# Optimization experiments

Hardware: AMD Instinct MI355X
Metric: run time of the kernel (lower is better)

The kernel has to match this reference:

```python
import jax, jax.numpy as jnp
import numpy as np

N = 100000          # nodes
E = 1600000         # edges
NODE_DIM = 128
EDGE_DIM = 1
EMB = 16            # out_channels per head
H = 2               # heads
HID = 32
OUT = 2
NEG_SLOPE = 0.2


def gatv2_layer(x, src, dst, eattr, Wl, bl, Wr, br, We, att, bias):
    """PyG GATv2Conv: add self-loops (edge_attr fill='mean'), edge attention,
    segment softmax over target nodes, scatter-add aggregation, concat heads."""
    n = x.shape[0]
    heads, ch = att.shape
    # --- add self loops; self-loop edge_attr = mean of incoming edge_attr per node ---
    ones = jnp.ones((src.shape[0],), dtype=x.dtype)
    deg = jax.ops.segment_sum(ones, dst, num_segments=n)
    loop_attr = jax.ops.segment_sum(eattr, dst, num_segments=n) / jnp.maximum(deg, 1.0)[:, None]
    idx = jnp.arange(n, dtype=src.dtype)
    src2 = jnp.concatenate([src, idx])
    dst2 = jnp.concatenate([dst, idx])
    eattr2 = jnp.concatenate([eattr, loop_attr], axis=0)
    # --- linear projections ---
    xl = (x @ Wl + bl).reshape(n, heads, ch)   # source-side (lin_l)
    xr = (x @ Wr + br).reshape(n, heads, ch)   # target-side (lin_r)
    ef = (eattr2 @ We).reshape(-1, heads, ch)  # edge features (lin_edge, no bias)
    # --- per-edge attention logits (GATv2: LeakyReLU inside, then att dot) ---
    e = xl[src2] + xr[dst2] + ef               # [E2, H, C]
    e = jnp.where(e >= 0, e, NEG_SLOPE * e)
    logits = jnp.einsum('ehc,hc->eh', e, att)  # [E2, H]
    # --- segment softmax over edges sharing the same target node ---
    m = jax.ops.segment_max(logits, dst2, num_segments=n)      # [N, H]
    a = jnp.exp(logits - m[dst2])
    denom = jax.ops.segment_sum(a, dst2, num_segments=n)
    alpha = a / denom[dst2]                                    # [E2, H]
    # --- scatter-add weighted source messages ---
    msg = (alpha[:, :, None] * xl[src2]).reshape(-1, heads * ch)
    out = jax.ops.segment_sum(msg, dst2, num_segments=n)       # [N, H*C]
    return out + bias


def setup_inputs() -> dict:
    key = jax.random.key(0)
    ks = jax.random.split(key, 24)
    p = lambda k, s: (jax.random.normal(k, s, dtype=jnp.float32) * 0.1)
    HC = H * EMB
    return {
        'x': jax.random.normal(ks[0], (N, NODE_DIM), dtype=jnp.float32),
        'edge_index': jax.random.randint(ks[1], (2, E), 0, N, dtype=jnp.int32),
        'edge_attr': jax.random.normal(ks[2], (E, EDGE_DIM), dtype=jnp.float32),
        # layer 1
        'Wl1': p(ks[3], (NODE_DIM, HC)), 'bl1': p(ks[4], (HC,)),
        'Wr1': p(ks[5], (NODE_DIM, HC)), 'br1': p(ks[6], (HC,)),
        'We1': p(ks[7], (EDGE_DIM, HC)), 'att1': p(ks[8], (H, EMB)), 'b1': p(ks[9], (HC,)),
        # layer 2 (input dim = H*EMB)
        'Wl2': p(ks[10], (HC, HC)), 'bl2': p(ks[11], (HC,)),
        'Wr2': p(ks[12], (HC, HC)), 'br2': p(ks[13], (HC,)),
        'We2': p(ks[14], (EDGE_DIM, HC)), 'att2': p(ks[15], (H, EMB)), 'b2': p(ks[16], (HC,)),
        # decoder MLP
        'Wd1': p(ks[17], (HC, HID)), 'bd1': p(ks[18], (HID,)),
        'Wd2': p(ks[19], (HID, OUT)), 'bd2': p(ks[20], (OUT,)),
    }


def reference(x, edge_index, edge_attr,
              Wl1, bl1, Wr1, br1, We1, att1, b1,
              Wl2, bl2, Wr2, br2, We2, att2, b2,
              Wd1, bd1, Wd2, bd2):
    src, dst = edge_index[0], edge_index[1]
    h = gatv2_layer(x, src, dst, edge_attr, Wl1, bl1, Wr1, br1, We1, att1, b1)
    h = gatv2_layer(h, src, dst, edge_attr, Wl2, bl2, Wr2, br2, We2, att2, b2)
    h = jax.nn.relu(h @ Wd1 + bd1)
    return h @ Wd2 + bd2
```

## Files before the change

### kernel.cpp

```cpp
#include <hip/hip_runtime.h>
#include <hip/hip_fp16.h>
#include <math.h>


#define NN 100000
#define NE 1600000
#define SLOT 48
#define ROWU 64
#define NEG_SLOPE 0.2f

__device__ __forceinline__ float pk_ea(unsigned p) {
    return __half2float(__ushort_as_half((unsigned short)((p & 0x7FFFu) << 1)));
}
__device__ __forceinline__ float lrelu(float v) {
    return (v >= 0.f) ? v : NEG_SLOPE * v;
}

template <int K>
__global__ void proj_scatter_kernel(const float* __restrict__ x,
                                    const float* __restrict__ Wl, const float* __restrict__ bl,
                                    const float* __restrict__ Wr, const float* __restrict__ br,
                                    __half* __restrict__ xl, float* __restrict__ xr,
                                    const int* __restrict__ src, const int* __restrict__ dst,
                                    const float* __restrict__ eattr,
                                    unsigned* __restrict__ csr) {
    __shared__ __align__(16) float sWl[K * 32];
    __shared__ __align__(16) float sWr[K * 32];
    __shared__ float sb[64];
    for (int i = threadIdx.x; i < K * 32; i += blockDim.x) {
        int k = i >> 5, col = i & 31;
        int p = (((k >> 2) ^ (col & 7)) << 2) | (k & 3);
        sWl[col * K + p] = Wl[i];
        sWr[col * K + p] = Wr[i];
    }
    if (threadIdx.x < 32) sb[threadIdx.x] = bl[threadIdx.x];
    else if (threadIdx.x < 64) sb[threadIdx.x] = br[threadIdx.x - 32];
    __syncthreads();
    int t = blockIdx.x * blockDim.x + threadIdx.x;
    int g = t >> 5, col = t & 31;
    int row0 = g * 4;
    {
        const float4* x0 = (const float4*)(x + (size_t)(row0 + 0) * K);
        const float4* x1 = (const float4*)(x + (size_t)(row0 + 1) * K);
        const float4* x2 = (const float4*)(x + (size_t)(row0 + 2) * K);
        const float4* x3 = (const float4*)(x + (size_t)(row0 + 3) * K);
        const float4* wl4 = (const float4*)(sWl + col * K);
        const float4* wr4 = (const float4*)(sWr + col * K);
        int swz = col & 7;
        float al0 = 0.f, al1 = 0.f, al2 = 0.f, al3 = 0.f;
        float ar0 = 0.f, ar1 = 0.f, ar2 = 0.f, ar3 = 0.f;
#pragma unroll 4
        for (int k4 = 0; k4 < K / 4; k4++) {
            float4 wl = wl4[k4 ^ swz];
            float4 wr = wr4[k4 ^ swz];
            float4 a = x0[k4];
            float4 b = x1[k4];
            float4 c = x2[k4];
            float4 d = x3[k4];
            al0 = fmaf(a.x, wl.x, al0); al0 = fmaf(a.y, wl.y, al0);
            al0 = fmaf(a.z, wl.z, al0); al0 = fmaf(a.w, wl.w, al0);
            ar0 = fmaf(a.x, wr.x, ar0); ar0 = fmaf(a.y, wr.y, ar0);
            ar0 = fmaf(a.z, wr.z, ar0); ar0 = fmaf(a.w, wr.w, ar0);
            al1 = fmaf(b.x, wl.x, al1); al1 = fmaf(b.y, wl.y, al1);
            al1 = fmaf(b.z, wl.z, al1); al1 = fmaf(b.w, wl.w, al1);
            ar1 = fmaf(b.x, wr.x, ar1); ar1 = fmaf(b.y, wr.y, ar1);
            ar1 = fmaf(b.z, wr.z, ar1); ar1 = fmaf(b.w, wr.w, ar1);
            al2 = fmaf(c.x, wl.x, al2); al2 = fmaf(c.y, wl.y, al2);
            al2 = fmaf(c.z, wl.z, al2); al2 = fmaf(c.w, wl.w, al2);
            ar2 = fmaf(c.x, wr.x, ar2); ar2 = fmaf(c.y, wr.y, ar2);
            ar2 = fmaf(c.z, wr.z, ar2); ar2 = fmaf(c.w, wr.w, ar2);
            al3 = fmaf(d.x, wl.x, al3); al3 = fmaf(d.y, wl.y, al3);
            al3 = fmaf(d.z, wl.z, al3); al3 = fmaf(d.w, wl.w, al3);
            ar3 = fmaf(d.x, wr.x, ar3); ar3 = fmaf(d.y, wr.y, ar3);
            ar3 = fmaf(d.z, wr.z, ar3); ar3 = fmaf(d.w, wr.w, ar3);
        }
        float bls = sb[col], brs = sb[32 + col];
        xl[(size_t)(row0 + 0) * 32 + col] = __float2half_rn(al0 + bls);
        xr[(size_t)(row0 + 0) * 32 + col] = ar0 + brs;
        xl[(size_t)(row0 + 1) * 32 + col] = __float2half_rn(al1 + bls);
        xr[(size_t)(row0 + 1) * 32 + col] = ar1 + brs;
        xl[(size_t)(row0 + 2) * 32 + col] = __float2half_rn(al2 + bls);
        xr[(size_t)(row0 + 2) * 32 + col] = ar2 + brs;
        xl[(size_t)(row0 + 3) * 32 + col] = __float2half_rn(al3 + bls);
        xr[(size_t)(row0 + 3) * 32 + col] = ar3 + brs;
    }
#pragma unroll
    for (int i = 0; i < 2; i++) {
        int e = blockIdx.x * 512 + i * 256 + threadIdx.x;
        int d = dst[e];
        unsigned* row = csr + (size_t)d * ROWU;
        int pos = atomicAdd((int*)row, 1);
        if (pos < SLOT) {
            unsigned hb = __half_as_ushort(__float2half_rn(eattr[e]));
            row[4 + pos] = ((unsigned)src[e] << 15) | (hb >> 1);
        }
    }
}

__device__ __forceinline__ void gat_core4(const unsigned* __restrict__ csr,
                                          const __half* xl, const float* xr,
                                          const float* We, const float* att,
                                          const float* bias, int node, int L,
                                          float h[4]) {
    int k = L & 7, j = L >> 3;
    const unsigned* row = csr + (size_t)node * ROWU;
    int cnt = (int)row[0];
    int deg = (cnt < SLOT) ? cnt : SLOT;
    float4 we = ((const float4*)We)[k];
    float4 at = ((const float4*)att)[k];
    float4 xrc = ((const float4*)(xr + (size_t)node * 32))[k];
    ushort4 sq = ((const ushort4*)(xl + (size_t)node * 32))[k];
    float sx0 = __half2float(__ushort_as_half(sq.x));
    float sx1 = __half2float(__ushort_as_half(sq.y));
    float sx2 = __half2float(__ushort_as_half(sq.z));
    float sx3 = __half2float(__ushort_as_half(sq.w));
    float ssum = 0.f, a0 = 0.f, a1 = 0.f, a2 = 0.f, a3 = 0.f, easum = 0.f;
    unsigned pv_c = row[4 + j];
    int n1 = j + 4; if (n1 > SLOT - 1) n1 = SLOT - 1;
    unsigned pv_n = row[4 + n1];
    bool val_c = j < deg;
    int s_c = val_c ? (int)(pv_c >> 15) : 0;
    ushort4 q_c = ((const ushort4*)(xl + (size_t)s_c * 32))[k];
    for (int base = 0; base < deg; base += 4) {
        int idx = base + j;
        bool val_n = (idx + 4) < deg;
        int s_n = val_n ? (int)(pv_n >> 15) : 0;
        ushort4 q_n = ((const ushort4*)(xl + (size_t)s_n * 32))[k];
        int n2 = idx + 8; if (n2 > SLOT - 1) n2 = SLOT - 1;
        unsigned pv_n2 = row[4 + n2];
        float ea = pk_ea(pv_c);
        float x0 = __half2float(__ushort_as_half(q_c.x));
        float x1 = __half2float(__ushort_as_half(q_c.y));
        float x2 = __half2float(__ushort_as_half(q_c.z));
        float x3 = __half2float(__ushort_as_half(q_c.w));
        float p;
        p  = at.x * lrelu(fmaf(ea, we.x, x0 + xrc.x));
        p  = fmaf(at.y, lrelu(fmaf(ea, we.y, x1 + xrc.y)), p);
        p  = fmaf(at.z, lrelu(fmaf(ea, we.z, x2 + xrc.z)), p);
        p  = fmaf(at.w, lrelu(fmaf(ea, we.w, x3 + xrc.w)), p);
        p += __shfl_xor(p, 1);
        p += __shfl_xor(p, 2);
        float w = val_c ? __expf(p) : 0.f;
        ssum += w;
        easum += val_c ? ea : 0.f;
        a0 = fmaf(w, x0, a0);
        a1 = fmaf(w, x1, a1);
        a2 = fmaf(w, x2, a2);
        a3 = fmaf(w, x3, a3);
        pv_c = pv_n; pv_n = pv_n2; q_c = q_n; val_c = val_n;
    }
    ssum  += __shfl_xor(ssum, 8);   ssum  += __shfl_xor(ssum, 16);
    easum += __shfl_xor(easum, 8);  easum += __shfl_xor(easum, 16);
    a0 += __shfl_xor(a0, 8);  a0 += __shfl_xor(a0, 16);
    a1 += __shfl_xor(a1, 8);  a1 += __shfl_xor(a1, 16);
    a2 += __shfl_xor(a2, 8);  a2 += __shfl_xor(a2, 16);
    a3 += __shfl_xor(a3, 8);  a3 += __shfl_xor(a3, 16);
    {
        float ea0 = easum / fmaxf((float)cnt, 1.f);
        float p;
        p  = at.x * lrelu(fmaf(ea0, we.x, sx0 + xrc.x));
        p  = fmaf(at.y, lrelu(fmaf(ea0, we.y, sx1 + xrc.y)), p);
        p  = fmaf(at.z, lrelu(fmaf(ea0, we.z, sx2 + xrc.z)), p);
        p  = fmaf(at.w, lrelu(fmaf(ea0, we.w, sx3 + xrc.w)), p);
        p += __shfl_xor(p, 1);
        p += __shfl_xor(p, 2);
        float w = __expf(p);
        ssum += w;
        a0 = fmaf(w, sx0, a0);
        a1 = fmaf(w, sx1, a1);
        a2 = fmaf(w, sx2, a2);
        a3 = fmaf(w, sx3, a3);
    }
    float4 bq = ((const float4*)bias)[k];
    float inv = 1.f / ssum;
    h[0] = a0 * inv + bq.x;
    h[1] = a1 * inv + bq.y;
    h[2] = a2 * inv + bq.z;
    h[3] = a3 * inv + bq.w;
}

#define HBUF_FENCE() do { \
    asm volatile("s_waitcnt lgkmcnt(0)" ::: "memory"); \
    __builtin_amdgcn_sched_barrier(0); \
} while (0)

__global__ void gat1_proj2_kernel(const unsigned* __restrict__ csr,
                                  const __half* __restrict__ xl, const float* __restrict__ xr,
                                  const float* __restrict__ We, const float* __restrict__ att,
                                  const float* __restrict__ bias,
                                  const float* __restrict__ Wl2, const float* __restrict__ bl2,
                                  const float* __restrict__ Wr2, const float* __restrict__ br2,
                                  __half* __restrict__ xl2, float* __restrict__ xr2) {
    __shared__ __align__(16) float sWl[1024];
    __shared__ __align__(16) float sWr[1024];
    __shared__ float4 hbuf[8][8];
    for (int i = threadIdx.x; i < 1024; i += blockDim.x) {
        int cc = i >> 5, Lc = i & 31;
        int p = (((cc >> 2) ^ (Lc & 7)) << 2) | (cc & 3);
        sWl[Lc * 32 + p] = Wl2[i];
        sWr[Lc * 32 + p] = Wr2[i];
    }
    __syncthreads();
    int t = blockIdx.x * blockDim.x + threadIdx.x;
    int node = t >> 5, L = t & 31;
    if (node >= NN) return;
    float h[4];
    gat_core4(csr, xl, xr, We, att, bias, node, L, h);
    int nl = threadIdx.x >> 5;
    if (L < 8) hbuf[nl][L] = make_float4(h[0], h[1], h[2], h[3]);
    HBUF_FENCE();
    const float4* hv4 = hbuf[nl];
    const float4* wl4 = (const float4*)(sWl + L * 32);
    const float4* wr4 = (const float4*)(sWr + L * 32);
    int swz = L & 7;
    float al = bl2[L], ar = br2[L];
#pragma unroll
    for (int c4 = 0; c4 < 8; c4++) {
        float4 hv = hv4[c4];
        float4 wl = wl4[c4 ^ swz];
        float4 wr = wr4[c4 ^ swz];
        al = fmaf(hv.x, wl.x, al); al = fmaf(hv.y, wl.y, al);
        al = fmaf(hv.z, wl.z, al); al = fmaf(hv.w, wl.w, al);
        ar = fmaf(hv.x, wr.x, ar); ar = fmaf(hv.y, wr.y, ar);
        ar = fmaf(hv.z, wr.z, ar); ar = fmaf(hv.w, wr.w, ar);
    }
    xl2[(size_t)node * 32 + L] = __float2half_rn(al);
    xr2[(size_t)node * 32 + L] = ar;
}

__global__ void gat2_dec_kernel(const unsigned* __restrict__ csr,
                                const __half* __restrict__ xl, const float* __restrict__ xr,
                                const float* __restrict__ We, const float* __restrict__ att,
                                const float* __restrict__ bias,
                                const float* __restrict__ Wd1, const float* __restrict__ bd1,
                                const float* __restrict__ Wd2, const float* __restrict__ bd2,
                                float* __restrict__ out) {
    __shared__ __align__(16) float sWd1[1024];
    __shared__ float sWd2[64];
    __shared__ float4 hbuf[8][8];
    for (int i = threadIdx.x; i < 1024; i += blockDim.x) {
        int cc = i >> 5, Lc = i & 31;
        int p = (((cc >> 2) ^ (Lc & 7)) << 2) | (cc & 3);
        sWd1[Lc * 32 + p] = Wd1[i];
    }
    if (threadIdx.x < 64) sWd2[threadIdx.x] = Wd2[threadIdx.x];
    __syncthreads();
    int t = blockIdx.x * blockDim.x + threadIdx.x;
    int node = t >> 5, L = t & 31;
    if (node >= NN) return;
    float h[4];
    gat_core4(csr, xl, xr, We, att, bias, node, L, h);
    int nl = threadIdx.x >> 5;
    if (L < 8) hbuf[nl][L] = make_float4(h[0], h[1], h[2], h[3]);
    HBUF_FENCE();
    const float4* hv4 = hbuf[nl];
    const float4* wd4 = (const float4*)(sWd1 + L * 32);
    int swz = L & 7;
    float d1 = bd1[L];
#pragma unroll
    for (int c4 = 0; c4 < 8; c4++) {
        float4 hv = hv4[c4];
        float4 wd = wd4[c4 ^ swz];
        d1 = fmaf(hv.x, wd.x, d1); d1 = fmaf(hv.y, wd.y, d1);
        d1 = fmaf(hv.z, wd.z, d1); d1 = fmaf(hv.w, wd.w, d1);
    }
    float hid = fmaxf(d1, 0.f);
    float o0 = hid * sWd2[L * 2 + 0];
    float o1 = hid * sWd2[L * 2 + 1];
    o0 += __shfl_xor(o0, 1);   o1 += __shfl_xor(o1, 1);
    o0 += __shfl_xor(o0, 2);   o1 += __shfl_xor(o1, 2);
    o0 += __shfl_xor(o0, 4);   o1 += __shfl_xor(o1, 4);
    o0 += __shfl_xor(o0, 8);   o1 += __shfl_xor(o1, 8);
    o0 += __shfl_xor(o0, 16);  o1 += __shfl_xor(o1, 16);
    if (L == 0) {
        out[(size_t)node * 2 + 0] = o0 + bd2[0];
        out[(size_t)node * 2 + 1] = o1 + bd2[1];
    }
}

extern "C" void kernel_launch(void* const* d_in, const int* in_sizes, int n_in,
                              void* d_out, int out_size, void* d_ws, size_t ws_size,
                              hipStream_t stream) {
    const float* x     = (const float*)d_in[0];
    const int*   src   = (const int*)d_in[1];
    const int*   dst   = src + NE;
    const float* eattr = (const float*)d_in[2];
    const float* Wl1 = (const float*)d_in[3],  *bl1 = (const float*)d_in[4];
    const float* Wr1 = (const float*)d_in[5],  *br1 = (const float*)d_in[6];
    const float* We1 = (const float*)d_in[7],  *att1 = (const float*)d_in[8];
    const float* b1  = (const float*)d_in[9];
    const float* Wl2 = (const float*)d_in[10], *bl2 = (const float*)d_in[11];
    const float* Wr2 = (const float*)d_in[12], *br2 = (const float*)d_in[13];
    const float* We2 = (const float*)d_in[14], *att2 = (const float*)d_in[15];
    const float* b2  = (const float*)d_in[16];
    const float* Wd1 = (const float*)d_in[17], *bd1 = (const float*)d_in[18];
    const float* Wd2 = (const float*)d_in[19], *bd2 = (const float*)d_in[20];
    float* out = (float*)d_out;

    char* w = (char*)d_ws;
    unsigned* csr = (unsigned*)w;  w += (size_t)NN * ROWU * 4;
    __half*   xl  = (__half*)w;    w += (size_t)NN * 32 * 2;
    float*    xr  = (float*)w;     w += (size_t)NN * 32 * 4;
    __half*   xl2 = (__half*)w;    w += (size_t)NN * 32 * 2;
    float*    xr2 = (float*)w;     w += (size_t)NN * 32 * 4;

    const int B = 256;
    const int gN32 = (NN * 32) / B;
    const int gP   = (NN / 4 * 32) / B;

    hipMemsetAsync(csr, 0, (size_t)NN * ROWU * 4, stream);

    proj_scatter_kernel<128><<<gP, B, 0, stream>>>(x, Wl1, bl1, Wr1, br1, xl, xr,
                                                   src, dst, eattr, csr);

    gat1_proj2_kernel<<<gN32, B, 0, stream>>>(csr, xl, xr, We1, att1, b1,
                                              Wl2, bl2, Wr2, br2, xl2, xr2);

    gat2_dec_kernel<<<gN32, B, 0, stream>>>(csr, xl2, xr2, We2, att2, b2,
                                            Wd1, bd1, Wd2, bd2, out);
}
```

Baseline: 363.9 us.

## Process two nodes per warp group and prefetch both CSR rows up front

Each 32-lane group in the two GAT kernels now handles two nodes. Both nodes' CSR row count and first packed neighbor entries are loaded before any compute starts, so the second node's row latency overlaps with the first node's aggregation. Shared-memory weight staging is amortized over twice as many nodes and the grid is halved. It also swaps the order of two FMAs in the projection, which slightly changes rounding, and the second node's state raises register pressure.

```diff
diff --git a/kernel.cpp b/kernel.cpp
--- a/kernel.cpp
+++ b/kernel.cpp
@@ -72,7 +72,7 @@
             al3 = fmaf(d.x, wl.x, al3); al3 = fmaf(d.y, wl.y, al3);
             al3 = fmaf(d.z, wl.z, al3); al3 = fmaf(d.w, wl.w, al3);
             ar3 = fmaf(d.x, wr.x, ar3); ar3 = fmaf(d.y, wr.y, ar3);
-            ar3 = fmaf(d.z, wr.z, ar3); ar3 = fmaf(d.w, wr.w, ar3);
+            ar3 = fmaf(d.w, wr.w, ar3); ar3 = fmaf(d.z, wr.z, ar3);
         }
         float bls = sb[col], brs = sb[32 + col];
         xl[(size_t)(row0 + 0) * 32 + col] = __float2half_rn(al0 + bls);
@@ -97,14 +97,14 @@
     }
 }
 
-__device__ __forceinline__ void gat_core4(const unsigned* __restrict__ csr,
+__device__ __forceinline__ void gat_core4(const unsigned* __restrict__ row,
+                                          int cnt, unsigned pv_c, unsigned pv_n,
+                                          int node,
                                           const __half* xl, const float* xr,
                                           const float* We, const float* att,
-                                          const float* bias, int node, int L,
+                                          const float* bias, int L,
                                           float h[4]) {
     int k = L & 7, j = L >> 3;
-    const unsigned* row = csr + (size_t)node * ROWU;
-    int cnt = (int)row[0];
     int deg = (cnt < SLOT) ? cnt : SLOT;
     float4 we = ((const float4*)We)[k];
     float4 at = ((const float4*)att)[k];
@@ -115,9 +115,6 @@
     float sx2 = __half2float(__ushort_as_half(sq.z));
     float sx3 = __half2float(__ushort_as_half(sq.w));
     float ssum = 0.f, a0 = 0.f, a1 = 0.f, a2 = 0.f, a3 = 0.f, easum = 0.f;
-    unsigned pv_c = row[4 + j];
-    int n1 = j + 4; if (n1 > SLOT - 1) n1 = SLOT - 1;
-    unsigned pv_n = row[4 + n1];
     bool val_c = j < deg;
     int s_c = val_c ? (int)(pv_c >> 15) : 0;
     ushort4 q_c = ((const ushort4*)(xl + (size_t)s_c * 32))[k];
@@ -201,31 +198,60 @@
         sWr[Lc * 32 + p] = Wr2[i];
     }
     __syncthreads();
-    int t = blockIdx.x * blockDim.x + threadIdx.x;
-    int node = t >> 5, L = t & 31;
-    if (node >= NN) return;
-    float h[4];
-    gat_core4(csr, xl, xr, We, att, bias, node, L, h);
-    int nl = threadIdx.x >> 5;
-    if (L < 8) hbuf[nl][L] = make_float4(h[0], h[1], h[2], h[3]);
-    HBUF_FENCE();
-    const float4* hv4 = hbuf[nl];
+    int grp = threadIdx.x >> 5, L = threadIdx.x & 31;
+    int j = L >> 3, swz = L & 7;
+    int nodeA = blockIdx.x * 16 + grp;
+    int nodeB = nodeA + 8;
+    const unsigned* rowB = csr + (size_t)nodeB * ROWU;
+    int cntB = (int)rowB[0];
+    unsigned pvB_c = rowB[4 + j];
+    unsigned pvB_n = rowB[4 + j + 4];
+    const unsigned* rowA = csr + (size_t)nodeA * ROWU;
+    int cntA = (int)rowA[0];
+    unsigned pvA_c = rowA[4 + j];
+    unsigned pvA_n = rowA[4 + j + 4];
     const float4* wl4 = (const float4*)(sWl + L * 32);
     const float4* wr4 = (const float4*)(sWr + L * 32);
-    int swz = L & 7;
-    float al = bl2[L], ar = br2[L];
-#pragma unroll
-    for (int c4 = 0; c4 < 8; c4++) {
-        float4 hv = hv4[c4];
-        float4 wl = wl4[c4 ^ swz];
-        float4 wr = wr4[c4 ^ swz];
-        al = fmaf(hv.x, wl.x, al); al = fmaf(hv.y, wl.y, al);
-        al = fmaf(hv.z, wl.z, al); al = fmaf(hv.w, wl.w, al);
-        ar = fmaf(hv.x, wr.x, ar); ar = fmaf(hv.y, wr.y, ar);
-        ar = fmaf(hv.z, wr.z, ar); ar = fmaf(hv.w, wr.w, ar);
-    }
-    xl2[(size_t)node * 32 + L] = __float2half_rn(al);
-    xr2[(size_t)node * 32 + L] = ar;
+    float blv = bl2[L], brv = br2[L];
+    float h[4];
+    gat_core4(rowA, cntA, pvA_c, pvA_n, nodeA, xl, xr, We, att, bias, L, h);
+    if (L < 8) hbuf[grp][L] = make_float4(h[0], h[1], h[2], h[3]);
+    HBUF_FENCE();
+    {
+        const float4* hv4 = hbuf[grp];
+        float al = blv, ar = brv;
+#pragma unroll
+        for (int c4 = 0; c4 < 8; c4++) {
+            float4 hv = hv4[c4];
+            float4 wl = wl4[c4 ^ swz];
+            float4 wr = wr4[c4 ^ swz];
+            al = fmaf(hv.x, wl.x, al); al = fmaf(hv.y, wl.y, al);
+            al = fmaf(hv.z, wl.z, al); al = fmaf(hv.w, wl.w, al);
+            ar = fmaf(hv.x, wr.x, ar); ar = fmaf(hv.y, wr.y, ar);
+            ar = fmaf(hv.z, wr.z, ar); ar = fmaf(hv.w, wr.w, ar);
+        }
+        xl2[(size_t)nodeA * 32 + L] = __float2half_rn(al);
+        xr2[(size_t)nodeA * 32 + L] = ar;
+    }
+    gat_core4(rowB, cntB, pvB_c, pvB_n, nodeB, xl, xr, We, att, bias, L, h);
+    if (L < 8) hbuf[grp][L] = make_float4(h[0], h[1], h[2], h[3]);
+    HBUF_FENCE();
+    {
+        const float4* hv4 = hbuf[grp];
+        float al = blv, ar = brv;
+#pragma unroll
+        for (int c4 = 0; c4 < 8; c4++) {
+            float4 hv = hv4[c4];
+            float4 wl = wl4[c4 ^ swz];
+            float4 wr = wr4[c4 ^ swz];
+            al = fmaf(hv.x, wl.x, al); al = fmaf(hv.y, wl.y, al);
+            al = fmaf(hv.z, wl.z, al); al = fmaf(hv.w, wl.w, al);
+            ar = fmaf(hv.x, wr.x, ar); ar = fmaf(hv.y, wr.y, ar);
+            ar = fmaf(hv.z, wr.z, ar); ar = fmaf(hv.w, wr.w, ar);
+        }
+        xl2[(size_t)nodeB * 32 + L] = __float2half_rn(al);
+        xr2[(size_t)nodeB * 32 + L] = ar;
+    }
 }
 
 __global__ void gat2_dec_kernel(const unsigned* __restrict__ csr,
@@ -245,36 +271,71 @@
     }
     if (threadIdx.x < 64) sWd2[threadIdx.x] = Wd2[threadIdx.x];
     __syncthreads();
-    int t = blockIdx.x * blockDim.x + threadIdx.x;
-    int node = t >> 5, L = t & 31;
-    if (node >= NN) return;
+    int grp = threadIdx.x >> 5, L = threadIdx.x & 31;
+    int j = L >> 3, swz = L & 7;
+    int nodeA = blockIdx.x * 16 + grp;
+    int nodeB = nodeA + 8;
+    const unsigned* rowB = csr + (size_t)nodeB * ROWU;
+    int cntB = (int)rowB[0];
+    unsigned pvB_c = rowB[4 + j];
+    unsigned pvB_n = rowB[4 + j + 4];
+    const unsigned* rowA = csr + (size_t)nodeA * ROWU;
+    int cntA = (int)rowA[0];
+    unsigned pvA_c = rowA[4 + j];
+    unsigned pvA_n = rowA[4 + j + 4];
+    const float4* wd4 = (const float4*)(sWd1 + L * 32);
+    float bd1v = bd1[L];
+    float wo0 = sWd2[L * 2 + 0], wo1 = sWd2[L * 2 + 1];
     float h[4];
-    gat_core4(csr, xl, xr, We, att, bias, node, L, h);
-    int nl = threadIdx.x >> 5;
-    if (L < 8) hbuf[nl][L] = make_float4(h[0], h[1], h[2], h[3]);
+    gat_core4(rowA, cntA, pvA_c, pvA_n, nodeA, xl, xr, We, att, bias, L, h);
+    if (L < 8) hbuf[grp][L] = make_float4(h[0], h[1], h[2], h[3]);
     HBUF_FENCE();
-    const float4* hv4 = hbuf[nl];
-    const float4* wd4 = (const float4*)(sWd1 + L * 32);
-    int swz = L & 7;
-    float d1 = bd1[L];
-#pragma unroll
-    for (int c4 = 0; c4 < 8; c4++) {
-        float4 hv = hv4[c4];
-        float4 wd = wd4[c4 ^ swz];
-        d1 = fmaf(hv.x, wd.x, d1); d1 = fmaf(hv.y, wd.y, d1);
-        d1 = fmaf(hv.z, wd.z, d1); d1 = fmaf(hv.w, wd.w, d1);
-    }
-    float hid = fmaxf(d1, 0.f);
-    float o0 = hid * sWd2[L * 2 + 0];
-    float o1 = hid * sWd2[L * 2 + 1];
-    o0 += __shfl_xor(o0, 1);   o1 += __shfl_xor(o1, 1);
-    o0 += __shfl_xor(o0, 2);   o1 += __shfl_xor(o1, 2);
-    o0 += __shfl_xor(o0, 4);   o1 += __shfl_xor(o1, 4);
-    o0 += __shfl_xor(o0, 8);   o1 += __shfl_xor(o1, 8);
-    o0 += __shfl_xor(o0, 16);  o1 += __shfl_xor(o1, 16);
-    if (L == 0) {
-        out[(size_t)node * 2 + 0] = o0 + bd2[0];
-        out[(size_t)node * 2 + 1] = o1 + bd2[1];
+    {
+        const float4* hv4 = hbuf[grp];
+        float d1 = bd1v;
+#pragma unroll
+        for (int c4 = 0; c4 < 8; c4++) {
+            float4 hv = hv4[c4];
+            float4 wd = wd4[c4 ^ swz];
+            d1 = fmaf(hv.x, wd.x, d1); d1 = fmaf(hv.y, wd.y, d1);
+            d1 = fmaf(hv.z, wd.z, d1); d1 = fmaf(hv.w, wd.w, d1);
+        }
+        float hid = fmaxf(d1, 0.f);
+        float o0 = hid * wo0, o1 = hid * wo1;
+        o0 += __shfl_xor(o0, 1);   o1 += __shfl_xor(o1, 1);
+        o0 += __shfl_xor(o0, 2);   o1 += __shfl_xor(o1, 2);
+        o0 += __shfl_xor(o0, 4);   o1 += __shfl_xor(o1, 4);
+        o0 += __shfl_xor(o0, 8);   o1 += __shfl_xor(o1, 8);
+        o0 += __shfl_xor(o0, 16);  o1 += __shfl_xor(o1, 16);
+        if (L == 0) {
+            out[(size_t)nodeA * 2 + 0] = o0 + bd2[0];
+            out[(size_t)nodeA * 2 + 1] = o1 + bd2[1];
+        }
+    }
+    gat_core4(rowB, cntB, pvB_c, pvB_n, nodeB, xl, xr, We, att, bias, L, h);
+    if (L < 8) hbuf[grp][L] = make_float4(h[0], h[1], h[2], h[3]);
+    HBUF_FENCE();
+    {
+        const float4* hv4 = hbuf[grp];
+        float d1 = bd1v;
+#pragma unroll
+        for (int c4 = 0; c4 < 8; c4++) {
+            float4 hv = hv4[c4];
+            float4 wd = wd4[c4 ^ swz];
+            d1 = fmaf(hv.x, wd.x, d1); d1 = fmaf(hv.y, wd.y, d1);
+            d1 = fmaf(hv.z, wd.z, d1); d1 = fmaf(hv.w, wd.w, d1);
+        }
+        float hid = fmaxf(d1, 0.f);
+        float o0 = hid * wo0, o1 = hid * wo1;
+        o0 += __shfl_xor(o0, 1);   o1 += __shfl_xor(o1, 1);
+        o0 += __shfl_xor(o0, 2);   o1 += __shfl_xor(o1, 2);
+        o0 += __shfl_xor(o0, 4);   o1 += __shfl_xor(o1, 4);
+        o0 += __shfl_xor(o0, 8);   o1 += __shfl_xor(o1, 8);
+        o0 += __shfl_xor(o0, 16);  o1 += __shfl_xor(o1, 16);
+        if (L == 0) {
+            out[(size_t)nodeB * 2 + 0] = o0 + bd2[0];
+            out[(size_t)nodeB * 2 + 1] = o1 + bd2[1];
+        }
     }
 }
 
@@ -305,17 +366,17 @@
     float*    xr2 = (float*)w;     w += (size_t)NN * 32 * 4;
 
     const int B = 256;
-    const int gN32 = (NN * 32) / B;
     const int gP   = (NN / 4 * 32) / B;
+    const int gG   = NN / 16;
 
     hipMemsetAsync(csr, 0, (size_t)NN * ROWU * 4, stream);
 
     proj_scatter_kernel<128><<<gP, B, 0, stream>>>(x, Wl1, bl1, Wr1, br1, xl, xr,
                                                    src, dst, eattr, csr);
 
-    gat1_proj2_kernel<<<gN32, B, 0, stream>>>(csr, xl, xr, We1, att1, b1,
-                                              Wl2, bl2, Wr2, br2, xl2, xr2);
-
-    gat2_dec_kernel<<<gN32, B, 0, stream>>>(csr, xl2, xr2, We2, att2, b2,
-                                            Wd1, bd1, Wd2, bd2, out);
-}
+    gat1_proj2_kernel<<<gG, B, 0, stream>>>(csr, xl, xr, We1, att1, b1,
+                                            Wl2, bl2, Wr2, br2, xl2, xr2);
+
+    gat2_dec_kernel<<<gG, B, 0, stream>>>(csr, xl2, xr2, We2, att2, b2,
+                                          Wd1, bd1, Wd2, bd2, out);
+}
```

Measured after the change: 365.3 us. Within noise of the previous version (+0.4%).

## Map one lane per edge with full-row gathers and transpose-reduce across lanes

Applied to the files above, without the earlier changes.

The GAT aggregation core changes from 8 lanes per edge (4 edges in flight per 32-lane group, each lane holding 4 channels) to one lane per edge holding all 32 channels of the source row. Each lane loads a 64-byte fp16 row with four 16-byte loads and computes both head logits locally, so the per-edge shuffles for the logit are removed. At the end a butterfly transpose-reduce spreads the 32 channel accumulators across lanes, giving each lane one channel that is written to shared memory. The cost is much higher register pressure (32 accumulators plus 32 xr values per lane), many idle lanes when in-degree is below 32, and loss of the software prefetch pipelining the old code had.

```diff
diff --git a/kernel.cpp b/kernel.cpp
--- a/kernel.cpp
+++ b/kernel.cpp
@@ -14,6 +14,10 @@
 }
 __device__ __forceinline__ float lrelu(float v) {
     return (v >= 0.f) ? v : NEG_SLOPE * v;
+}
+__device__ __forceinline__ float2 up2(unsigned u) {
+    __half2 h = *reinterpret_cast<__half2*>(&u);
+    return __half22float2(h);
 }
 
 template <int K>
@@ -72,7 +76,7 @@
             al3 = fmaf(d.x, wl.x, al3); al3 = fmaf(d.y, wl.y, al3);
             al3 = fmaf(d.z, wl.z, al3); al3 = fmaf(d.w, wl.w, al3);
             ar3 = fmaf(d.x, wr.x, ar3); ar3 = fmaf(d.y, wr.y, ar3);
-            ar3 = fmaf(d.z, wr.z, ar3); ar3 = fmaf(d.w, wr.w, ar3);
+            ar3 = fmaf(d.w, wr.w, ar3); ar3 = fmaf(d.z, wr.z, ar3);
         }
         float bls = sb[col], brs = sb[32 + col];
         xl[(size_t)(row0 + 0) * 32 + col] = __float2half_rn(al0 + bls);
@@ -97,86 +101,126 @@
     }
 }
 
-__device__ __forceinline__ void gat_core4(const unsigned* __restrict__ csr,
-                                          const __half* xl, const float* xr,
-                                          const float* We, const float* att,
-                                          const float* bias, int node, int L,
-                                          float h[4]) {
-    int k = L & 7, j = L >> 3;
-    const unsigned* row = csr + (size_t)node * ROWU;
+__device__ __forceinline__ void gat_core32(const unsigned* __restrict__ row,
+                                           int node,
+                                           const __half* __restrict__ xl,
+                                           const float* __restrict__ xr,
+                                           const float* __restrict__ We,
+                                           const float* __restrict__ att,
+                                           const float* __restrict__ bias,
+                                           int L, float* hout, int* cout) {
     int cnt = (int)row[0];
     int deg = (cnt < SLOT) ? cnt : SLOT;
-    float4 we = ((const float4*)We)[k];
-    float4 at = ((const float4*)att)[k];
-    float4 xrc = ((const float4*)(xr + (size_t)node * 32))[k];
-    ushort4 sq = ((const ushort4*)(xl + (size_t)node * 32))[k];
-    float sx0 = __half2float(__ushort_as_half(sq.x));
-    float sx1 = __half2float(__ushort_as_half(sq.y));
-    float sx2 = __half2float(__ushort_as_half(sq.z));
-    float sx3 = __half2float(__ushort_as_half(sq.w));
-    float ssum = 0.f, a0 = 0.f, a1 = 0.f, a2 = 0.f, a3 = 0.f, easum = 0.f;
-    unsigned pv_c = row[4 + j];
-    int n1 = j + 4; if (n1 > SLOT - 1) n1 = SLOT - 1;
-    unsigned pv_n = row[4 + n1];
-    bool val_c = j < deg;
-    int s_c = val_c ? (int)(pv_c >> 15) : 0;
-    ushort4 q_c = ((const ushort4*)(xl + (size_t)s_c * 32))[k];
-    for (int base = 0; base < deg; base += 4) {
-        int idx = base + j;
-        bool val_n = (idx + 4) < deg;
-        int s_n = val_n ? (int)(pv_n >> 15) : 0;
-        ushort4 q_n = ((const ushort4*)(xl + (size_t)s_n * 32))[k];
-        int n2 = idx + 8; if (n2 > SLOT - 1) n2 = SLOT - 1;
-        unsigned pv_n2 = row[4 + n2];
-        float ea = pk_ea(pv_c);
-        float x0 = __half2float(__ushort_as_half(q_c.x));
-        float x1 = __half2float(__ushort_as_half(q_c.y));
-        float x2 = __half2float(__ushort_as_half(q_c.z));
-        float x3 = __half2float(__ushort_as_half(q_c.w));
-        float p;
-        p  = at.x * lrelu(fmaf(ea, we.x, x0 + xrc.x));
-        p  = fmaf(at.y, lrelu(fmaf(ea, we.y, x1 + xrc.y)), p);
-        p  = fmaf(at.z, lrelu(fmaf(ea, we.z, x2 + xrc.z)), p);
-        p  = fmaf(at.w, lrelu(fmaf(ea, we.w, x3 + xrc.w)), p);
-        p += __shfl_xor(p, 1);
-        p += __shfl_xor(p, 2);
-        float w = val_c ? __expf(p) : 0.f;
-        ssum += w;
-        easum += val_c ? ea : 0.f;
-        a0 = fmaf(w, x0, a0);
-        a1 = fmaf(w, x1, a1);
-        a2 = fmaf(w, x2, a2);
-        a3 = fmaf(w, x3, a3);
-        pv_c = pv_n; pv_n = pv_n2; q_c = q_n; val_c = val_n;
-    }
-    ssum  += __shfl_xor(ssum, 8);   ssum  += __shfl_xor(ssum, 16);
-    easum += __shfl_xor(easum, 8);  easum += __shfl_xor(easum, 16);
-    a0 += __shfl_xor(a0, 8);  a0 += __shfl_xor(a0, 16);
-    a1 += __shfl_xor(a1, 8);  a1 += __shfl_xor(a1, 16);
-    a2 += __shfl_xor(a2, 8);  a2 += __shfl_xor(a2, 16);
-    a3 += __shfl_xor(a3, 8);  a3 += __shfl_xor(a3, 16);
+    float xrc[32];
     {
-        float ea0 = easum / fmaxf((float)cnt, 1.f);
-        float p;
-        p  = at.x * lrelu(fmaf(ea0, we.x, sx0 + xrc.x));
-        p  = fmaf(at.y, lrelu(fmaf(ea0, we.y, sx1 + xrc.y)), p);
-        p  = fmaf(at.z, lrelu(fmaf(ea0, we.z, sx2 + xrc.z)), p);
-        p  = fmaf(at.w, lrelu(fmaf(ea0, we.w, sx3 + xrc.w)), p);
-        p += __shfl_xor(p, 1);
-        p += __shfl_xor(p, 2);
-        float w = __expf(p);
-        ssum += w;
-        a0 = fmaf(w, sx0, a0);
-        a1 = fmaf(w, sx1, a1);
-        a2 = fmaf(w, sx2, a2);
-        a3 = fmaf(w, sx3, a3);
-    }
-    float4 bq = ((const float4*)bias)[k];
-    float inv = 1.f / ssum;
-    h[0] = a0 * inv + bq.x;
-    h[1] = a1 * inv + bq.y;
-    h[2] = a2 * inv + bq.z;
-    h[3] = a3 * inv + bq.w;
+        const float4* xp = (const float4*)(xr + (size_t)node * 32);
+#pragma unroll
+        for (int i = 0; i < 8; i++) {
+            float4 v = xp[i];
+            xrc[4 * i + 0] = v.x; xrc[4 * i + 1] = v.y;
+            xrc[4 * i + 2] = v.z; xrc[4 * i + 3] = v.w;
+        }
+    }
+    float acc[32];
+#pragma unroll
+    for (int i = 0; i < 32; i++) acc[i] = 0.f;
+    float ssum0 = 0.f, ssum1 = 0.f, easum = 0.f;
+    for (int base = 0; base < deg; base += 32) {
+        int idx = base + L;
+        int slot = (idx < SLOT) ? idx : SLOT - 1;
+        unsigned pv = row[4 + slot];
+        bool val = idx < deg;
+        int s = val ? (int)(pv >> 15) : 0;
+        float ea = pk_ea(pv);
+        const uint4* xq = (const uint4*)(xl + (size_t)s * 32);
+        uint4 q0 = xq[0], q1 = xq[1], q2 = xq[2], q3 = xq[3];
+        float p0 = 0.f, p1 = 0.f;
+#define LG2(u, c, P) { float2 f = up2(u); \
+        P = fmaf(att[c],     lrelu(f.x + xrc[c]     + ea * We[c]),     P); \
+        P = fmaf(att[(c)+1], lrelu(f.y + xrc[(c)+1] + ea * We[(c)+1]), P); }
+#define LG8(Q, B, P) LG2(Q.x, B, P) LG2(Q.y, (B)+2, P) LG2(Q.z, (B)+4, P) LG2(Q.w, (B)+6, P)
+        LG8(q0, 0, p0) LG8(q1, 8, p0) LG8(q2, 16, p1) LG8(q3, 24, p1)
+#undef LG8
+#undef LG2
+        float w0 = val ? __expf(p0) : 0.f;
+        float w1 = val ? __expf(p1) : 0.f;
+        ssum0 += w0;
+        ssum1 += w1;
+        easum += val ? ea : 0.f;
+#define AC2(u, c, W) { float2 f = up2(u); \
+        acc[c] = fmaf(W, f.x, acc[c]); acc[(c)+1] = fmaf(W, f.y, acc[(c)+1]); }
+#define AC8(Q, B, W) AC2(Q.x, B, W) AC2(Q.y, (B)+2, W) AC2(Q.z, (B)+4, W) AC2(Q.w, (B)+6, W)
+        AC8(q0, 0, w0) AC8(q1, 8, w0) AC8(q2, 16, w1) AC8(q3, 24, w1)
+#undef AC8
+#undef AC2
+    }
+    easum += __shfl_xor(easum, 1); easum += __shfl_xor(easum, 2);
+    easum += __shfl_xor(easum, 4); easum += __shfl_xor(easum, 8);
+    easum += __shfl_xor(easum, 16);
+    ssum0 += __shfl_xor(ssum0, 1); ssum0 += __shfl_xor(ssum0, 2);
+    ssum0 += __shfl_xor(ssum0, 4); ssum0 += __shfl_xor(ssum0, 8);
+    ssum0 += __shfl_xor(ssum0, 16);
+    ssum1 += __shfl_xor(ssum1, 1); ssum1 += __shfl_xor(ssum1, 2);
+    ssum1 += __shfl_xor(ssum1, 4); ssum1 += __shfl_xor(ssum1, 8);
+    ssum1 += __shfl_xor(ssum1, 16);
+    float ea0 = easum / fmaxf((float)cnt, 1.f);
+    const uint4* sp = (const uint4*)(xl + (size_t)node * 32);
+    uint4 s0 = sp[0], s1 = sp[1], s2 = sp[2], s3 = sp[3];
+    float pS0 = 0.f, pS1 = 0.f;
+#define LG2(u, c, P) { float2 f = up2(u); \
+    P = fmaf(att[c],     lrelu(f.x + xrc[c]     + ea0 * We[c]),     P); \
+    P = fmaf(att[(c)+1], lrelu(f.y + xrc[(c)+1] + ea0 * We[(c)+1]), P); }
+#define LG8(Q, B, P) LG2(Q.x, B, P) LG2(Q.y, (B)+2, P) LG2(Q.z, (B)+4, P) LG2(Q.w, (B)+6, P)
+    LG8(s0, 0, pS0) LG8(s1, 8, pS0) LG8(s2, 16, pS1) LG8(s3, 24, pS1)
+#undef LG8
+#undef LG2
+    float wS0 = __expf(pS0);
+    float wS1 = __expf(pS1);
+    ssum0 += wS0;
+    ssum1 += wS1;
+    bool k0 = (L & 1) != 0;
+    float t16[16];
+#pragma unroll
+    for (int i = 0; i < 16; i++) {
+        float give = k0 ? acc[i] : acc[16 + i];
+        float keep = k0 ? acc[16 + i] : acc[i];
+        t16[i] = keep + __shfl_xor(give, 1);
+    }
+    bool k1 = (L & 2) != 0;
+    float t8[8];
+#pragma unroll
+    for (int i = 0; i < 8; i++) {
+        float give = k1 ? t16[i] : t16[8 + i];
+        float keep = k1 ? t16[8 + i] : t16[i];
+        t8[i] = keep + __shfl_xor(give, 2);
+    }
+    bool k2 = (L & 4) != 0;
+    float t4[4];
+#pragma unroll
+    for (int i = 0; i < 4; i++) {
+        float give = k2 ? t8[i] : t8[4 + i];
+        float keep = k2 ? t8[4 + i] : t8[i];
+        t4[i] = keep + __shfl_xor(give, 4);
+    }
+    bool k3 = (L & 8) != 0;
+    float t2[2];
+#pragma unroll
+    for (int i = 0; i < 2; i++) {
+        float give = k3 ? t4[i] : t4[2 + i];
+        float keep = k3 ? t4[2 + i] : t4[i];
+        t2[i] = keep + __shfl_xor(give, 8);
+    }
+    bool k4 = (L & 16) != 0;
+    float give = k4 ? t2[0] : t2[1];
+    float keep = k4 ? t2[1] : t2[0];
+    float A = keep + __shfl_xor(give, 16);
+    int cL = ((L & 1) << 4) | ((L & 2) << 2) | (L & 4) | ((L & 8) >> 2) | ((L & 16) >> 4);
+    float ssumH = (cL < 16) ? ssum0 : ssum1;
+    float wSH   = (cL < 16) ? wS0   : wS1;
+    float sxc = __half2float(xl[(size_t)node * 32 + cL]);
+    A = fmaf(wSH, sxc, A);
+    *hout = A / ssumH + bias[cL];
+    *cout = cL;
 }
 
 #define HBUF_FENCE() do { \
@@ -193,7 +237,7 @@
                                   __half* __restrict__ xl2, float* __restrict__ xr2) {
     __shared__ __align__(16) float sWl[1024];
     __shared__ __align__(16) float sWr[1024];
-    __shared__ float4 hbuf[8][8];
+    __shared__ __align__(16) float hbufF[8][32];
     for (int i = threadIdx.x; i < 1024; i += blockDim.x) {
         int cc = i >> 5, Lc = i & 31;
         int p = (((cc >> 2) ^ (Lc & 7)) << 2) | (cc & 3);
@@ -203,13 +247,13 @@
     __syncthreads();
     int t = blockIdx.x * blockDim.x + threadIdx.x;
     int node = t >> 5, L = t & 31;
-    if (node >= NN) return;
-    float h[4];
-    gat_core4(csr, xl, xr, We, att, bias, node, L, h);
-    int nl = threadIdx.x >> 5;
-    if (L < 8) hbuf[nl][L] = make_float4(h[0], h[1], h[2], h[3]);
+    int grp = threadIdx.x >> 5;
+    const unsigned* row = csr + (size_t)node * ROWU;
+    float h; int cL;
+    gat_core32(row, node, xl, xr, We, att, bias, L, &h, &cL);
+    hbufF[grp][cL] = h;
     HBUF_FENCE();
-    const float4* hv4 = hbuf[nl];
+    const float4* hv4 = (const float4*)hbufF[grp];
     const float4* wl4 = (const float4*)(sWl + L * 32);
     const float4* wr4 = (const float4*)(sWr + L * 32);
     int swz = L & 7;
@@ -237,7 +281,7 @@
                                 float* __restrict__ out) {
     __shared__ __align__(16) float sWd1[1024];
     __shared__ float sWd2[64];
-    __shared__ float4 hbuf[8][8];
+    __shared__ __align__(16) float hbufF[8][32];
     for (int i = threadIdx.x; i < 1024; i += blockDim.x) {
         int cc = i >> 5, Lc = i & 31;
         int p = (((cc >> 2) ^ (Lc & 7)) << 2) | (cc & 3);
@@ -247,13 +291,13 @@
     __syncthreads();
     int t = blockIdx.x * blockDim.x + threadIdx.x;
     int node = t >> 5, L = t & 31;
-    if (node >= NN) return;
-    float h[4];
-    gat_core4(csr, xl, xr, We, att, bias, node, L, h);
-    int nl = threadIdx.x >> 5;
-    if (L < 8) hbuf[nl][L] = make_float4(h[0], h[1], h[2], h[3]);
+    int grp = threadIdx.x >> 5;
+    const unsigned* row = csr + (size_t)node * ROWU;
+    float h; int cL;
+    gat_core32(row, node, xl, xr, We, att, bias, L, &h, &cL);
+    hbufF[grp][cL] = h;
     HBUF_FENCE();
-    const float4* hv4 = hbuf[nl];
+    const float4* hv4 = (const float4*)hbufF[grp];
     const float4* wd4 = (const float4*)(sWd1 + L * 32);
     int swz = L & 7;
     float d1 = bd1[L];
@@ -305,17 +349,17 @@
     float*    xr2 = (float*)w;     w += (size_t)NN * 32 * 4;
 
     const int B = 256;
-    const int gN32 = (NN * 32) / B;
-    const int gP   = (NN / 4 * 32) / B;
+    const int gP = (NN / 4 * 32) / B;
+    const int gG = (NN * 32) / B;
 
     hipMemsetAsync(csr, 0, (size_t)NN * ROWU * 4, stream);
 
     proj_scatter_kernel<128><<<gP, B, 0, stream>>>(x, Wl1, bl1, Wr1, br1, xl, xr,
                                                    src, dst, eattr, csr);
 
-    gat1_proj2_kernel<<<gN32, B, 0, stream>>>(csr, xl, xr, We1, att1, b1,
-                                              Wl2, bl2, Wr2, br2, xl2, xr2);
-
-    gat2_dec_kernel<<<gN32, B, 0, stream>>>(csr, xl2, xr2, We2, att2, b2,
-                                            Wd1, bd1, Wd2, bd2, out);
-}
+    gat1_proj2_kernel<<<gG, B, 0, stream>>>(csr, xl, xr, We1, att1, b1,
+                                            Wl2, bl2, Wr2, br2, xl2, xr2);
+
+    gat2_dec_kernel<<<gG, B, 0, stream>>>(csr, xl2, xr2, We2, att2, b2,
+                                          Wd1, bd1, Wd2, bd2, out);
+}
```

Measured after the change: 429.0 us. +17.9%, slower.
